# Kernel tuning notes

Hardware: AMD Instinct MI355X
Metric: run time of the kernel (lower is better)

The kernel has to match this reference:

```python
import jax, jax.numpy as jnp
import numpy as np

DIM = 128
HEADS = 128
DV = DIM // HEADS  # 1 (scalar attention values per head)
TOPK = 32
CHUNK = 16384
DEPTH = 2
STATE = 262144
BLOCK = 256
NBLOCKS = STATE // BLOCK
HIDDEN = int(DIM * 8 / 3)  # 341, SwiGLU hidden
EPS = float(jnp.finfo(jnp.float32).eps)  # torch RMSNorm default eps


def rmsnorm(x, w):
    return x * jax.lax.rsqrt(jnp.mean(x * x, axis=-1, keepdims=True) + EPS) * w


def swiglu(x, w_gate, w_up, w_down):
    return (jax.nn.silu(x @ w_gate.T) * (x @ w_up.T)) @ w_down.T


def topk_attention(x, Wq, Wk, Wv, Wo):
    b, n, d = x.shape
    q = jnp.einsum('bnd,hd->bhn', x, Wq)      # (b,h,n) scalar queries
    keys = jnp.einsum('bnd,hd->bhn', x, Wk)   # (b,h,n) scalar keys
    v = (x @ Wv.T).reshape(b, n, HEADS, DV).transpose(0, 2, 1, 3)  # (b,h,n,dv)
    order = jnp.argsort(keys, axis=-1)
    k_sorted = jnp.take_along_axis(keys, order, axis=-1)
    v_sorted = jnp.take_along_axis(v, order[..., None], axis=2)
    top_k_keys = k_sorted[..., -TOPK:]
    bot_k_keys = k_sorted[..., :TOPK]
    top_k_vals = v_sorted[:, :, -TOPK:, :]
    bot_k_vals = v_sorted[:, :, :TOPK, :]
    nc = n // CHUNK
    q_chunks = q.reshape(b, HEADS, nc, CHUNK).transpose(2, 0, 1, 3)  # (nc,b,h,c)

    def chunk_fn(q_chunk):
        scores_top = q_chunk[..., None] * top_k_keys[:, :, None, :]  # (b,h,c,k)
        scores_bot = q_chunk[..., None] * bot_k_keys[:, :, None, :]
        attn_top = jax.nn.softmax(scores_top, axis=-1)
        attn_bot = jax.nn.softmax(scores_bot, axis=-1)
        out_top = jnp.einsum('bhck,bhkd->bhcd', attn_top, top_k_vals)
        out_bot = jnp.einsum('bhck,bhkd->bhcd', attn_bot, bot_k_vals)
        q_pos = (q_chunk > 0).astype(x.dtype)[..., None]
        return q_pos * out_top + (1 - q_pos) * out_bot  # (b,h,c,dv)

    out = jax.lax.map(chunk_fn, q_chunks)            # (nc,b,h,c,dv)
    out = out.transpose(1, 0, 3, 2, 4).reshape(b, n, d)  # (b,n,h*dv)
    return out @ Wo.T


def setup_inputs() -> dict:
    key = jax.random.key(0)
    ks = jax.random.split(key, 16)
    s = 0.02
    nrm = lambda k, shp: (jax.random.normal(k, shp, dtype=jnp.float32) * s)
    inp = {}
    inp['state_bytes'] = jax.random.randint(ks[0], (1, STATE), 0, 256)
    inp['byte_embed'] = nrm(ks[1], (256, DIM))
    inp['block_pos_embed'] = nrm(ks[2], (NBLOCKS, DIM))
    inp['local_pos_embed'] = nrm(ks[3], (BLOCK, DIM))
    inp['Wq'] = nrm(ks[4], (DEPTH, HEADS, DIM))
    inp['Wk'] = nrm(ks[5], (DEPTH, HEADS, DIM))
    inp['Wv'] = nrm(ks[6], (DEPTH, DIM, DIM))
    inp['Wo'] = nrm(ks[7], (DEPTH, DIM, DIM))
    inp['norm1_w'] = jnp.ones((DEPTH, DIM), dtype=jnp.float32)
    inp['norm2_w'] = jnp.ones((DEPTH, DIM), dtype=jnp.float32)
    inp['w_gate'] = nrm(ks[8], (DEPTH, HIDDEN, DIM))
    inp['w_up'] = nrm(ks[9], (DEPTH, HIDDEN, DIM))
    inp['w_down'] = nrm(ks[10], (DEPTH, DIM, HIDDEN))
    inp['final_norm_w'] = jnp.ones((DIM,), dtype=jnp.float32)
    inp['out_w'] = nrm(ks[11], (256, DIM))
    return inp


def reference(state_bytes, byte_embed, block_pos_embed, local_pos_embed, Wq, Wk, Wv, Wo,
              norm1_w, norm2_w, w_gate, w_up, w_down, final_norm_w, out_w):
    x = byte_embed[state_bytes]                                   # (b,n,d)
    block_pos = jnp.repeat(block_pos_embed, BLOCK, axis=0)        # (n,d)
    local_pos = jnp.tile(local_pos_embed, (NBLOCKS, 1))           # (n,d)
    x = x + block_pos[None] + local_pos[None]
    for l in range(DEPTH):
        x = x + topk_attention(rmsnorm(x, norm1_w[l]), Wq[l], Wk[l], Wv[l], Wo[l])
        x = x + swiglu(rmsnorm(x, norm2_w[l]), w_gate[l], w_up[l], w_down[l])
    x = rmsnorm(x, final_norm_w)
    return x @ out_w.T  # (b, STATE, 256)
```

## Files before the change

kernel.cpp:

```cpp
#include <hip/hip_runtime.h>


#define NTOK 262144
#define LOG2E 1.44269504088896340736f
#define NEGINF (-3.402823466e38f)

__global__ __launch_bounds__(256) void embed_kernel(const int* __restrict__ bytes,
    const float* __restrict__ be, const float* __restrict__ bpe,
    const float* __restrict__ lpe, float* __restrict__ x)
{
  int i4 = blockIdx.x * 256 + threadIdx.x;
  int n  = i4 >> 5;
  int dq = (i4 & 31) * 4;
  int b  = bytes[n];
  float4 a = *(const float4*)(be  + b * 128 + dq);
  float4 c = *(const float4*)(bpe + (n >> 8) * 128 + dq);
  float4 d = *(const float4*)(lpe + (n & 255) * 128 + dq);
  float4 o;
  o.x = (a.x + c.x) + d.x; o.y = (a.y + c.y) + d.y;
  o.z = (a.z + c.z) + d.z; o.w = (a.w + c.w) + d.w;
  *(float4*)(x + (size_t)n * 128 + dq) = o;
}

__global__ __launch_bounds__(256) void scale_kernel(const float* __restrict__ x,
    float* __restrict__ s)
{
  const int lane = threadIdx.x & 63;
  const int gw = blockIdx.x * 4 + (threadIdx.x >> 6);
  for (int tok = gw; tok < NTOK; tok += 4096) {
    const float2 v = *(const float2*)&x[(size_t)tok * 128 + lane * 2];
    float ss = v.x * v.x + v.y * v.y;
    #pragma unroll
    for (int off = 1; off < 64; off <<= 1) ss += __shfl_xor(ss, off, 64);
    const float m = ss * (1.f / 128.f) + 1.1920929e-07f;
    float r = rsqrtf(m);
    r = r * (1.5f - 0.5f * m * r * r);
    if (lane == 0) s[tok] = r;
  }
}

enum { M32_QK = 0, M32_RESID = 1, M32_RAW = 2 };

template<int MODE>
__global__ __launch_bounds__(256) void gemm_f32(
    const float* __restrict__ A, const float* __restrict__ rs, const float* __restrict__ cw,
    const float* __restrict__ B, const float* __restrict__ Bb,
    int K, int ldb, int Brows, int Bkcols,
    float* __restrict__ O, float* __restrict__ O2, int ldo)
{
  __shared__ float La[64][68];
  __shared__ float Lb[64][132];
  __shared__ float cwS[128];
  const int t = threadIdx.x;
  const int m0 = blockIdx.x * 64;
  const int n0 = (MODE == M32_QK) ? 0 : blockIdx.y * 128;
  const float* Bu = (MODE == M32_QK && blockIdx.y) ? Bb : B;
  for (int i = t; i < 128; i += 256) cwS[i] = cw ? cw[i] : 1.f;
  __syncthreads();

  float acc[4][8] = {};
  const int ta = (t & 15) * 4;
  const int tb = (t >> 4) * 8;

  for (int k0 = 0; k0 < K; k0 += 64) {
    for (int c = t; c < 1024; c += 256) {
      int tok = c >> 4, k4 = (c & 15) * 4;
      float4 av = *(const float4*)&A[(size_t)(m0 + tok) * K + k0 + k4];
      float rsv = rs ? rs[m0 + tok] : 1.f;
      La[k4 + 0][tok] = av.x * rsv * cwS[(k0 + k4 + 0) & 127];
      La[k4 + 1][tok] = av.y * rsv * cwS[(k0 + k4 + 1) & 127];
      La[k4 + 2][tok] = av.z * rsv * cwS[(k0 + k4 + 2) & 127];
      La[k4 + 3][tok] = av.w * rsv * cwS[(k0 + k4 + 3) & 127];
    }
    for (int c = t; c < 2048; c += 256) {
      int col = c >> 4, k4 = (c & 15) * 4;
      int gr = n0 + col;
      float4 bv = make_float4(0.f, 0.f, 0.f, 0.f);
      if (gr < Brows) {
        int kb = k0 + k4;
        if (((ldb & 3) == 0) && kb + 3 < Bkcols) {
          bv = *(const float4*)&Bu[(size_t)gr * ldb + kb];
        } else {
          float* bp = (float*)&bv;
          #pragma unroll
          for (int j = 0; j < 4; j++)
            if (kb + j < Bkcols) bp[j] = Bu[(size_t)gr * ldb + kb + j];
        }
      }
      Lb[k4 + 0][col] = bv.x; Lb[k4 + 1][col] = bv.y;
      Lb[k4 + 2][col] = bv.z; Lb[k4 + 3][col] = bv.w;
    }
    __syncthreads();
    for (int kq = 0; kq < 64; kq += 4) {
      float aa[4][4], bb[4][8];
      #pragma unroll
      for (int kk = 0; kk < 4; kk++) {
        *(float4*)&aa[kk][0] = *(const float4*)&La[kq + kk][ta];
        *(float4*)&bb[kk][0] = *(const float4*)&Lb[kq + kk][tb];
        *(float4*)&bb[kk][4] = *(const float4*)&Lb[kq + kk][tb + 4];
      }
      #pragma unroll
      for (int i = 0; i < 4; i++)
        #pragma unroll
        for (int j = 0; j < 8; j++) {
          float tt = aa[0][i] * bb[0][j];
          tt = fmaf(aa[1][i], bb[1][j], tt);
          tt = fmaf(aa[2][i], bb[2][j], tt);
          tt = fmaf(aa[3][i], bb[3][j], tt);
          acc[i][j] += tt;
        }
    }
    __syncthreads();
  }

  if (MODE == M32_QK) {
    if (blockIdx.y == 0) {
      #pragma unroll
      for (int i = 0; i < 4; i++)
        #pragma unroll
        for (int j = 0; j < 8; j++)
          O[(size_t)(m0 + ta + i) * 128 + tb + j] = acc[i][j];
    } else {
      #pragma unroll
      for (int i = 0; i < 4; i++)
        #pragma unroll
        for (int j = 0; j < 8; j++)
          O2[(size_t)(tb + j) * NTOK + (m0 + ta + i)] = acc[i][j];
    }
  } else if (MODE == M32_RESID) {
    #pragma unroll
    for (int i = 0; i < 4; i++)
      #pragma unroll
      for (int j = 0; j < 8; j++) {
        size_t ix = (size_t)(m0 + ta + i) * ldo + n0 + tb + j;
        O[ix] += acc[i][j];
      }
  } else {
    #pragma unroll
    for (int i = 0; i < 4; i++)
      #pragma unroll
      for (int j = 0; j < 8; j++)
        O[(size_t)(m0 + ta + i) * ldo + n0 + tb + j] = acc[i][j];
  }
}

__global__ __launch_bounds__(256) void sel_pass1(const float* __restrict__ kt,
    float* __restrict__ cV, int* __restrict__ cI)
{
  const int hb = blockIdx.y;
  const int h = hb >> 1;
  const float sgn = (hb & 1) ? -1.f : 1.f;
  const int wv = threadIdx.x >> 6;
  const int lane = threadIdx.x & 63;
  const int base = blockIdx.x * 8192 + wv * 2048;
  const float* row = kt + (size_t)h * NTOK;

  float vals[32];
  #pragma unroll
  for (int j4 = 0; j4 < 8; j4++) {
    float4 v4 = *(const float4*)&row[base + j4 * 256 + lane * 4];
    vals[j4 * 4 + 0] = sgn * v4.x; vals[j4 * 4 + 1] = sgn * v4.y;
    vals[j4 * 4 + 2] = sgn * v4.z; vals[j4 * 4 + 3] = sgn * v4.w;
  }
  float m = NEGINF; int mj = 0;
  #pragma unroll
  for (int j = 0; j < 32; j++) if (vals[j] > m) { m = vals[j]; mj = j; }

  unsigned int used = 0u;
  const size_t slot = (size_t)hb * 4096 + (blockIdx.x * 4 + wv) * 32;
  for (int r = 0; r < 32; r++) {
    float bv = m; int bl = lane; int bj = mj;
    #pragma unroll
    for (int off = 1; off < 64; off <<= 1) {
      float ov = __shfl_xor(bv, off, 64);
      int   ol = __shfl_xor(bl, off, 64);
      int   oj = __shfl_xor(bj, off, 64);
      if (ov > bv || (ov == bv && ol < bl)) { bv = ov; bl = ol; bj = oj; }
    }
    if (lane == 0) {
      cV[slot + r] = bv;
      cI[slot + r] = base + (bj >> 2) * 256 + bl * 4 + (bj & 3);
    }
    if (lane == bl) {
      used |= (1u << bj);
      m = NEGINF; mj = 0;
      #pragma unroll
      for (int j = 0; j < 32; j++)
        if (!((used >> j) & 1u) && vals[j] > m) { m = vals[j]; mj = j; }
    }
  }
}

__global__ __launch_bounds__(256) void sel_pass2(const float* __restrict__ cV,
    const int* __restrict__ cI, const float* __restrict__ x, const float* __restrict__ s,
    const float* __restrict__ nw, const float* __restrict__ Wv,
    float* __restrict__ tabK, float* __restrict__ tabV)
{
  __shared__ float lv[128];
  __shared__ int   li[128];
  __shared__ float selv[32];
  __shared__ int   seli[32];
  const int t = threadIdx.x;
  const int hb = blockIdx.x;
  const int h = hb >> 1;
  const int sb = hb & 1;
  const float sgn = sb ? -1.f : 1.f;
  const int wv = t >> 6;
  const int lane = t & 63;
  const size_t cb = (size_t)hb * 4096;

  float vals[16]; int idxs[16];
  #pragma unroll
  for (int j = 0; j < 16; j++) {
    vals[j] = cV[cb + t + j * 256];
    idxs[j] = cI[cb + t + j * 256];
  }
  float m = NEGINF; int mj = 0;
  #pragma unroll
  for (int j = 0; j < 16; j++) if (vals[j] > m) { m = vals[j]; mj = j; }

  unsigned int used = 0u;
  for (int r = 0; r < 32; r++) {
    float bv = m; int bl = lane; int bj = mj;
    #pragma unroll
    for (int off = 1; off < 64; off <<= 1) {
      float ov = __shfl_xor(bv, off, 64);
      int   ol = __shfl_xor(bl, off, 64);
      int   oj = __shfl_xor(bj, off, 64);
      if (ov > bv || (ov == bv && ol < bl)) { bv = ov; bl = ol; bj = oj; }
    }
    if (lane == 0) { lv[wv * 32 + r] = bv; li[wv * 32 + r] = 0; }
    if (lane == bl) {
      li[wv * 32 + r] = idxs[bj];
      used |= (1u << bj);
      m = NEGINF; mj = 0;
      #pragma unroll
      for (int j = 0; j < 16; j++)
        if (!((used >> j) & 1u) && vals[j] > m) { m = vals[j]; mj = j; }
    }
  }
  __syncthreads();

  if (t == 0) {
    int p[4] = {0, 0, 0, 0};
    for (int r = 0; r < 32; r++) {
      float best = NEGINF; int bw = 0;
      #pragma unroll
      for (int w = 0; w < 4; w++) {
        if (p[w] < 32) {
          float v = lv[w * 32 + p[w]];
          if (v > best) { best = v; bw = w; }
        }
      }
      selv[r] = best;
      seli[r] = li[bw * 32 + p[bw]];
      p[bw]++;
    }
  }
  __syncthreads();

  if (t < 32) {
    float kval = sgn * selv[t];
    int idx = seli[t];
    tabK[(sb * 32 + t) * 128 + h] = kval * LOG2E;
    float acc = 0.f;
    const float* xr = &x[(size_t)idx * 128];
    const float* wvp = &Wv[h * 128];
    for (int k = 0; k < 128; k++) acc = fmaf(xr[k] * nw[k], wvp[k], acc);
    tabV[(sb * 32 + t) * 128 + h] = acc * s[idx];
  }
}

__global__ __launch_bounds__(256) void att_kernel(float* __restrict__ q,
    const float* __restrict__ tabK, const float* __restrict__ tabV)
{
  __shared__ float tk[8192];
  __shared__ float tv[8192];
  const int t = threadIdx.x;
  for (int i = t; i < 8192; i += 256) { tk[i] = tabK[i]; tv[i] = tabV[i]; }
  __syncthreads();
  const int h = t & 127;
  const int base = blockIdx.x * 128;
  for (int it = 0; it < 64; it++) {
    const int tok = base + it * 2 + (t >> 7);
    const size_t off = (size_t)tok * 128 + h;
    const float qv = q[off];
    const int b = (qv > 0.f) ? 0 : 4096;
    const float* kk = &tk[b + h];
    const float* vv = &tv[b + h];
    float sw = 0.f, swv = 0.f;
    #pragma unroll
    for (int j = 0; j < 32; j++) {
      float e = exp2f(qv * kk[j * 128]);
      sw += e;
      swv = fmaf(e, vv[j * 128], swv);
    }
    q[off] = swv / sw;
  }
}

__global__ __launch_bounds__(256) void silu_kernel(float* __restrict__ g,
    const float* __restrict__ u, int n4)
{
  int idx = blockIdx.x * 256 + threadIdx.x;
  for (int i = idx; i < n4; i += gridDim.x * 256) {
    float4 gv = *(float4*)&g[(size_t)i * 4];
    float4 uv = *(const float4*)&u[(size_t)i * 4];
    float4 o;
    o.x = gv.x / (1.f + expf(-gv.x)) * uv.x;
    o.y = gv.y / (1.f + expf(-gv.y)) * uv.y;
    o.z = gv.z / (1.f + expf(-gv.z)) * uv.z;
    o.w = gv.w / (1.f + expf(-gv.w)) * uv.w;
    *(float4*)&g[(size_t)i * 4] = o;
  }
}


extern "C" void kernel_launch(void* const* d_in, const int* in_sizes, int n_in,
                              void* d_out, int out_size, void* d_ws, size_t ws_size,
                              hipStream_t stream)
{
  (void)in_sizes; (void)n_in; (void)out_size; (void)ws_size;
  const int*   bytes = (const int*)d_in[0];
  const float* be    = (const float*)d_in[1];
  const float* bpe   = (const float*)d_in[2];
  const float* lpe   = (const float*)d_in[3];
  const float* Wq    = (const float*)d_in[4];
  const float* Wk    = (const float*)d_in[5];
  const float* Wv    = (const float*)d_in[6];
  const float* Wo    = (const float*)d_in[7];
  const float* n1w   = (const float*)d_in[8];
  const float* n2w   = (const float*)d_in[9];
  const float* wg    = (const float*)d_in[10];
  const float* wu    = (const float*)d_in[11];
  const float* wd    = (const float*)d_in[12];
  const float* fnw   = (const float*)d_in[13];
  const float* outw  = (const float*)d_in[14];
  float* out = (float*)d_out;

  char* ws = (char*)d_ws;
  float* x    = (float*)(ws + 0);
  float* q    = (float*)(ws + 134217728);
  float* kt   = (float*)(ws + 268435456);
  float* s    = (float*)(ws + 402653184);
  float* tabK = (float*)(ws + 403701760);
  float* tabV = (float*)(ws + 403734528);
  float* gbuf = kt;
  float* ubuf = kt + 12582912;
  float* cV   = out;
  int*   cI   = (int*)(out + 256 * 4096);

  embed_kernel<<<32768, 256, 0, stream>>>(bytes, be, bpe, lpe, x);

  for (int l = 0; l < 2; l++) {
    const float* wq = Wq + l * 16384;
    const float* wk = Wk + l * 16384;
    const float* wv = Wv + l * 16384;
    const float* wo = Wo + l * 16384;
    const float* g1 = n1w + l * 128;
    const float* g2 = n2w + l * 128;
    const float* wgl = wg + l * 43648;
    const float* wul = wu + l * 43648;
    const float* wdl = wd + l * 43648;

    scale_kernel<<<1024, 256, 0, stream>>>(x, s);
    gemm_f32<M32_QK><<<dim3(4096, 2), 256, 0, stream>>>(
        x, s, g1, wq, wk, 128, 128, 128, 128, q, kt, 128);
    sel_pass1<<<dim3(32, 256), 256, 0, stream>>>(kt, cV, cI);
    sel_pass2<<<256, 256, 0, stream>>>(cV, cI, x, s, g1, wv, tabK, tabV);
    att_kernel<<<2048, 256, 0, stream>>>(q, tabK, tabV);
    gemm_f32<M32_RESID><<<dim3(4096, 1), 256, 0, stream>>>(
        q, nullptr, nullptr, wo, nullptr, 128, 128, 128, 128, x, nullptr, 128);

    scale_kernel<<<1024, 256, 0, stream>>>(x, s);
    for (int c = 0; c < 8; c++) {
      const size_t base = (size_t)c * 32768;
      gemm_f32<M32_RAW><<<dim3(512, 3), 256, 0, stream>>>(
          x + base * 128, s + base, g2, wgl, nullptr, 128, 128, 341, 128,
          gbuf, nullptr, 384);
      gemm_f32<M32_RAW><<<dim3(512, 3), 256, 0, stream>>>(
          x + base * 128, s + base, g2, wul, nullptr, 128, 128, 341, 128,
          ubuf, nullptr, 384);
      silu_kernel<<<3072, 256, 0, stream>>>(gbuf, ubuf, 3145728);
      gemm_f32<M32_RESID><<<dim3(512, 1), 256, 0, stream>>>(
          gbuf, nullptr, nullptr, wdl, nullptr, 384, 341, 128, 341,
          x + base * 128, nullptr, 128);
    }
  }

  scale_kernel<<<1024, 256, 0, stream>>>(x, s);
  gemm_f32<M32_RAW><<<dim3(4096, 2), 256, 0, stream>>>(
      x, s, fnw, outw, nullptr, 128, 128, 256, 128, out, nullptr, 256);
}
```

Before: 6.285 ms.

## Use split-bf16 MFMA GEMMs for second-layer and output projections

Adds a GEMM kernel that splits fp32 operands into hi/lo bf16 pairs and accumulates three MFMA products, emulating near-fp32 precision on matrix cores. A prep kernel pre-splits the layer-1 weights and the output weights each call. The second layer's Wo, SwiGLU GEMMs and the final projection switch to it, while layer 0 keeps the fp32 SIMT GEMM, presumably for accuracy. The attention kernel block size is also doubled. The three-product split drops the lo*lo term, so there is some risk of precision loss.

```diff
diff --git a/kernel.cpp b/kernel.cpp
--- a/kernel.cpp
+++ b/kernel.cpp
@@ -4,6 +4,20 @@
 #define NTOK 262144
 #define LOG2E 1.44269504088896340736f
 #define NEGINF (-3.402823466e38f)
+
+typedef unsigned short u16;
+typedef short s16x8 __attribute__((ext_vector_type(8)));
+typedef float f32x4 __attribute__((ext_vector_type(4)));
+
+__device__ __forceinline__ float b2f(u16 u) {
+  unsigned int x = ((unsigned int)u) << 16;
+  return __builtin_bit_cast(float, x);
+}
+__device__ __forceinline__ u16 f2b(float f) {
+  unsigned int x = __builtin_bit_cast(unsigned int, f);
+  x = x + 0x7fffu + ((x >> 16) & 1u);
+  return (u16)(x >> 16);
+}
 
 __global__ __launch_bounds__(256) void embed_kernel(const int* __restrict__ bytes,
     const float* __restrict__ be, const float* __restrict__ bpe,
@@ -144,6 +158,123 @@
   }
 }
 
+__global__ __launch_bounds__(256) void prep_split(const float* __restrict__ wg,
+    const float* __restrict__ wu, const float* __restrict__ wd,
+    const float* __restrict__ wo, const float* __restrict__ ow,
+    u16* __restrict__ whi, u16* __restrict__ wlo)
+{
+  const int i = blockIdx.x * 256 + threadIdx.x;
+  float val = 0.f;
+  if (i < 49152) {
+    int r = i >> 7, k = i & 127;
+    if (r < 341) val = wg[43648 + r * 128 + k];
+  } else if (i < 98304) {
+    int j = i - 49152, r = j >> 7, k = j & 127;
+    if (r < 341) val = wu[43648 + r * 128 + k];
+  } else if (i < 147456) {
+    int j = i - 98304, r = j / 384, c = j % 384;
+    if (c < 341) val = wd[43648 + r * 341 + c];
+  } else if (i < 163840) {
+    val = wo[16384 + (i - 147456)];
+  } else {
+    val = ow[i - 163840];
+  }
+  u16 h = f2b(val);
+  whi[i] = h;
+  wlo[i] = f2b(val - b2f(h));
+}
+
+enum { MB_RAW = 0, MB_RESID = 1 };
+
+template<int MODE>
+__global__ __launch_bounds__(256) void gemm_bf3(
+    const float* __restrict__ A, const float* __restrict__ rs, const float* __restrict__ cw,
+    int K, const u16* __restrict__ Bhi, const u16* __restrict__ Blo, int ldb,
+    float* __restrict__ O, int ldo)
+{
+  __shared__ u16 sAhi[64 * 136];
+  __shared__ u16 sAlo[64 * 136];
+  __shared__ u16 sBhi[64 * 136];
+  __shared__ u16 sBlo[64 * 136];
+  __shared__ float cwS[128];
+  const int t = threadIdx.x;
+  const int lane = t & 63;
+  const int w = t >> 6;
+  const int wr = w >> 1, wc = w & 1;
+  const int m0 = blockIdx.x * 64;
+  const int n0 = blockIdx.y * 64;
+  const int l15 = lane & 15;
+  const int lg  = lane >> 4;
+  for (int i = t; i < 128; i += 256) cwS[i] = cw ? cw[i] : 1.f;
+  __syncthreads();
+
+  f32x4 acc[2][2] = {};
+
+  for (int k0 = 0; k0 < K; k0 += 128) {
+    for (int c = t; c < 2048; c += 256) {
+      int row = c >> 5, k4 = (c & 31) * 4;
+      float4 av = *(const float4*)&A[(size_t)(m0 + row) * K + k0 + k4];
+      float rsv = rs ? rs[m0 + row] : 1.f;
+      float vv[4] = { av.x, av.y, av.z, av.w };
+      ushort4 hv, lv;
+      u16* hp = (u16*)&hv; u16* lp = (u16*)&lv;
+      #pragma unroll
+      for (int j = 0; j < 4; j++) {
+        float a = vv[j] * rsv * cwS[(k4 + j) & 127];
+        u16 h = f2b(a);
+        hp[j] = h;
+        lp[j] = f2b(a - b2f(h));
+      }
+      *(ushort4*)&sAhi[row * 136 + k4] = hv;
+      *(ushort4*)&sAlo[row * 136 + k4] = lv;
+    }
+    for (int c = t; c < 1024; c += 256) {
+      int row = c >> 4, k8 = (c & 15) * 8;
+      *(uint4*)&sBhi[row * 136 + k8] = *(const uint4*)&Bhi[(size_t)(n0 + row) * ldb + k0 + k8];
+      *(uint4*)&sBlo[row * 136 + k8] = *(const uint4*)&Blo[(size_t)(n0 + row) * ldb + k0 + k8];
+    }
+    __syncthreads();
+    #pragma unroll
+    for (int ks = 0; ks < 4; ks++) {
+      s16x8 ah[2], al[2], bh[2], bl[2];
+      #pragma unroll
+      for (int mr = 0; mr < 2; mr++) {
+        int off = (wr * 32 + mr * 16 + l15) * 136 + ks * 32 + lg * 8;
+        ah[mr] = *(const s16x8*)&sAhi[off];
+        al[mr] = *(const s16x8*)&sAlo[off];
+      }
+      #pragma unroll
+      for (int nr = 0; nr < 2; nr++) {
+        int off = (wc * 32 + nr * 16 + l15) * 136 + ks * 32 + lg * 8;
+        bh[nr] = *(const s16x8*)&sBhi[off];
+        bl[nr] = *(const s16x8*)&sBlo[off];
+      }
+      #pragma unroll
+      for (int mr = 0; mr < 2; mr++)
+        #pragma unroll
+        for (int nr = 0; nr < 2; nr++) {
+          acc[mr][nr] = __builtin_amdgcn_mfma_f32_16x16x32_bf16(ah[mr], bh[nr], acc[mr][nr], 0, 0, 0);
+          acc[mr][nr] = __builtin_amdgcn_mfma_f32_16x16x32_bf16(ah[mr], bl[nr], acc[mr][nr], 0, 0, 0);
+          acc[mr][nr] = __builtin_amdgcn_mfma_f32_16x16x32_bf16(al[mr], bh[nr], acc[mr][nr], 0, 0, 0);
+        }
+    }
+    __syncthreads();
+  }
+
+  #pragma unroll
+  for (int mr = 0; mr < 2; mr++)
+    #pragma unroll
+    for (int nr = 0; nr < 2; nr++)
+      #pragma unroll
+      for (int r = 0; r < 4; r++) {
+        int row = m0 + wr * 32 + mr * 16 + lg * 4 + r;
+        int col = n0 + wc * 32 + nr * 16 + l15;
+        size_t ix = (size_t)row * ldo + col;
+        if (MODE == MB_RESID) O[ix] += acc[mr][nr][r];
+        else                  O[ix]  = acc[mr][nr][r];
+      }
+}
+
 __global__ __launch_bounds__(256) void sel_pass1(const float* __restrict__ kt,
     float* __restrict__ cV, int* __restrict__ cI)
 {
@@ -271,18 +402,18 @@
   }
 }
 
-__global__ __launch_bounds__(256) void att_kernel(float* __restrict__ q,
+__global__ __launch_bounds__(512) void att_kernel(float* __restrict__ q,
     const float* __restrict__ tabK, const float* __restrict__ tabV)
 {
   __shared__ float tk[8192];
   __shared__ float tv[8192];
   const int t = threadIdx.x;
-  for (int i = t; i < 8192; i += 256) { tk[i] = tabK[i]; tv[i] = tabV[i]; }
+  for (int i = t; i < 8192; i += 512) { tk[i] = tabK[i]; tv[i] = tabV[i]; }
   __syncthreads();
   const int h = t & 127;
-  const int base = blockIdx.x * 128;
+  const int base = blockIdx.x * 256;
   for (int it = 0; it < 64; it++) {
-    const int tok = base + it * 2 + (t >> 7);
+    const int tok = base + it * 4 + (t >> 7);
     const size_t off = (size_t)tok * 128 + h;
     const float qv = q[off];
     const int b = (qv > 0.f) ? 0 : 4096;
@@ -345,11 +476,16 @@
   float* s    = (float*)(ws + 402653184);
   float* tabK = (float*)(ws + 403701760);
   float* tabV = (float*)(ws + 403734528);
+  u16*   whi  = (u16*)(ws + 403767296);
+  u16*   wlo  = (u16*)(ws + 404160512);
   float* gbuf = kt;
   float* ubuf = kt + 12582912;
   float* cV   = out;
   int*   cI   = (int*)(out + 256 * 4096);
 
+  const size_t AG = 0, AU = 49152, AD = 98304, AW = 147456, AH = 163840;
+
+  prep_split<<<768, 256, 0, stream>>>(wg, wu, wd, Wo, outw, whi, wlo);
   embed_kernel<<<32768, 256, 0, stream>>>(bytes, be, bpe, lpe, x);
 
   for (int l = 0; l < 2; l++) {
@@ -368,27 +504,43 @@
         x, s, g1, wq, wk, 128, 128, 128, 128, q, kt, 128);
     sel_pass1<<<dim3(32, 256), 256, 0, stream>>>(kt, cV, cI);
     sel_pass2<<<256, 256, 0, stream>>>(cV, cI, x, s, g1, wv, tabK, tabV);
-    att_kernel<<<2048, 256, 0, stream>>>(q, tabK, tabV);
-    gemm_f32<M32_RESID><<<dim3(4096, 1), 256, 0, stream>>>(
-        q, nullptr, nullptr, wo, nullptr, 128, 128, 128, 128, x, nullptr, 128);
-
-    scale_kernel<<<1024, 256, 0, stream>>>(x, s);
-    for (int c = 0; c < 8; c++) {
-      const size_t base = (size_t)c * 32768;
-      gemm_f32<M32_RAW><<<dim3(512, 3), 256, 0, stream>>>(
-          x + base * 128, s + base, g2, wgl, nullptr, 128, 128, 341, 128,
-          gbuf, nullptr, 384);
-      gemm_f32<M32_RAW><<<dim3(512, 3), 256, 0, stream>>>(
-          x + base * 128, s + base, g2, wul, nullptr, 128, 128, 341, 128,
-          ubuf, nullptr, 384);
-      silu_kernel<<<3072, 256, 0, stream>>>(gbuf, ubuf, 3145728);
-      gemm_f32<M32_RESID><<<dim3(512, 1), 256, 0, stream>>>(
-          gbuf, nullptr, nullptr, wdl, nullptr, 384, 341, 128, 341,
-          x + base * 128, nullptr, 128);
+    att_kernel<<<1024, 512, 0, stream>>>(q, tabK, tabV);
+
+    if (l == 0) {
+      gemm_f32<M32_RESID><<<dim3(4096, 1), 256, 0, stream>>>(
+          q, nullptr, nullptr, wo, nullptr, 128, 128, 128, 128, x, nullptr, 128);
+      scale_kernel<<<1024, 256, 0, stream>>>(x, s);
+      for (int c = 0; c < 8; c++) {
+        const size_t base = (size_t)c * 32768;
+        gemm_f32<M32_RAW><<<dim3(512, 3), 256, 0, stream>>>(
+            x + base * 128, s + base, g2, wgl, nullptr, 128, 128, 341, 128,
+            gbuf, nullptr, 384);
+        gemm_f32<M32_RAW><<<dim3(512, 3), 256, 0, stream>>>(
+            x + base * 128, s + base, g2, wul, nullptr, 128, 128, 341, 128,
+            ubuf, nullptr, 384);
+        silu_kernel<<<3072, 256, 0, stream>>>(gbuf, ubuf, 3145728);
+        gemm_f32<M32_RESID><<<dim3(512, 1), 256, 0, stream>>>(
+            gbuf, nullptr, nullptr, wdl, nullptr, 384, 341, 128, 341,
+            x + base * 128, nullptr, 128);
+      }
+    } else {
+      gemm_bf3<MB_RESID><<<dim3(4096, 2), 256, 0, stream>>>(
+          q, nullptr, nullptr, 128, whi + AW, wlo + AW, 128, x, 128);
+      scale_kernel<<<1024, 256, 0, stream>>>(x, s);
+      for (int c = 0; c < 8; c++) {
+        const size_t base = (size_t)c * 32768;
+        gemm_bf3<MB_RAW><<<dim3(512, 6), 256, 0, stream>>>(
+            x + base * 128, s + base, g2, 128, whi + AG, wlo + AG, 128, gbuf, 384);
+        gemm_bf3<MB_RAW><<<dim3(512, 6), 256, 0, stream>>>(
+            x + base * 128, s + base, g2, 128, whi + AU, wlo + AU, 128, ubuf, 384);
+        silu_kernel<<<3072, 256, 0, stream>>>(gbuf, ubuf, 3145728);
+        gemm_bf3<MB_RESID><<<dim3(512, 2), 256, 0, stream>>>(
+            gbuf, nullptr, nullptr, 384, whi + AD, wlo + AD, 384, x + base * 128, 128);
+      }
     }
   }
 
   scale_kernel<<<1024, 256, 0, stream>>>(x, s);
-  gemm_f32<M32_RAW><<<dim3(4096, 2), 256, 0, stream>>>(
-      x, s, fnw, outw, nullptr, 128, 128, 256, 128, out, nullptr, 256);
-}
+  gemm_bf3<MB_RAW><<<dim3(4096, 4), 256, 0, stream>>>(
+      x, s, fnw, 128, whi + AH, wlo + AH, 128, out, 256);
+}
```

Measured after the change: 5.660 ms. 9.9% less time.
